# Kernel optimization log

Hardware: AMD Instinct MI355X
Metric: run time of the kernel (lower is better)

The kernel has to match this reference:

```python
import jax, jax.numpy as jnp
import numpy as np

V, D, DU, H = 50000, 256, 1024, 128
TEMP = 0.01

def time_cosine_emb(t, d_model):
    half = d_model // 2
    div_term = jnp.exp(jnp.arange(half, dtype=jnp.float32) * (-np.log(10000.0) / half))
    scaled = t[..., None] * div_term  # (B, L, half)
    return jnp.concatenate([jnp.sin(scaled), jnp.cos(scaled)], axis=-1)

def setup_inputs() -> dict:
    key = jax.random.key(0)
    ks = jax.random.split(key, 12)
    B, L = 64, 2048
    q_seq = jax.random.randint(ks[0], (B, L), 0, V)
    r_seq = jax.random.randint(ks[1], (B, L), 0, 3)
    t_seq = jax.random.uniform(ks[2], (B, L), dtype=jnp.float32) * 1000.0
    mask = jnp.ones((B, L), dtype=jnp.float32)
    q_tab = jax.random.normal(ks[3], (V, D), dtype=jnp.float32) * 0.02
    q_tab = q_tab.at[0].set(0.0)  # padding_idx=0
    r_tab = jax.random.normal(ks[4], (3, D), dtype=jnp.float32) * 0.02
    r_tab = r_tab.at[0].set(0.0)  # padding_idx=0
    virtual_node = jax.random.normal(ks[5], (1, D), dtype=jnp.float32)
    Ws1 = jax.random.normal(ks[6], (H, 2 * D), dtype=jnp.float32) * (1.0 / np.sqrt(2 * D))
    bs1 = jnp.zeros((H,), dtype=jnp.float32)
    Ws2 = jax.random.normal(ks[7], (1, H), dtype=jnp.float32) * (1.0 / np.sqrt(H))
    bs2 = jnp.zeros((1,), dtype=jnp.float32)
    Wa = jax.random.normal(ks[8], (DU, D), dtype=jnp.float32) * (1.0 / np.sqrt(D))
    ba = jnp.zeros((DU,), dtype=jnp.float32)
    return {"q_seq": q_seq, "r_seq": r_seq, "t_seq": t_seq, "mask": mask,
            "q_tab": q_tab, "r_tab": r_tab, "virtual_node": virtual_node,
            "Ws1": Ws1, "bs1": bs1, "Ws2": Ws2, "bs2": bs2, "Wa": Wa, "ba": ba}

def reference(q_seq, r_seq, t_seq, mask, q_tab, r_tab, virtual_node, Ws1, bs1, Ws2, bs2, Wa, ba):
    B, L = q_seq.shape
    d_model = q_tab.shape[1]
    # embedding gathers + trig time embedding
    h_events = q_tab[q_seq] + r_tab[r_seq] + time_cosine_emb(t_seq, d_model)  # (B,L,D)
    h_virtual = jnp.broadcast_to(virtual_node[None, :, :], (B, L, d_model))
    pair = jnp.concatenate([h_events, h_virtual], axis=-1)  # (B,L,2D)
    # struct_head: Linear -> LeakyReLU(0.2) -> Linear
    hdn = jax.nn.leaky_relu(jnp.einsum('bld,hd->blh', pair, Ws1) + bs1, 0.2)
    logits = jnp.einsum('blh,oh->blo', hdn, Ws2) + bs2  # (B,L,1)
    A_hat = jax.nn.sigmoid(logits / TEMP) * mask[..., None]
    # aggregator: Linear -> LeakyReLU(0.2)
    h_trans = jax.nn.leaky_relu(jnp.einsum('bld,ud->blu', h_events, Wa) + ba, 0.2)  # (B,L,DU)
    u_i = jnp.sum(h_trans * A_hat, axis=1)  # (B,DU)
    return (u_i, jnp.squeeze(A_hat, -1))
```

## Files before the change

kernel.cpp:

```cpp
#include <hip/hip_runtime.h>

typedef unsigned short ushort_t;
typedef unsigned int uint_t;

typedef short bf16x8 __attribute__((ext_vector_type(8)));
typedef float f32x4 __attribute__((ext_vector_type(4)));

#define MFMA16(a, b, c) __builtin_amdgcn_mfma_f32_16x16x32_bf16(a, b, c, 0, 0, 0)

__device__ __forceinline__ ushort_t f2bf(float f) {
    uint_t u = __float_as_uint(f);
    u += 0x7fffu + ((u >> 16) & 1u);
    return (ushort_t)(u >> 16);
}
__device__ __forceinline__ float bf2f(ushort_t h) {
    return __uint_as_float(((uint_t)h) << 16);
}

__device__ __forceinline__ void async16(const ushort_t* g, ushort_t* l) {
    __builtin_amdgcn_global_load_lds(
        (const __attribute__((address_space(1))) uint_t*)g,
        (__attribute__((address_space(3))) uint_t*)l, 16, 0, 0);
}

__global__ void k_prep(const float* __restrict__ Ws1, const float* __restrict__ bs1,
                       const float* __restrict__ virt, const float* __restrict__ Wa,
                       float* __restrict__ consth, ushort_t* __restrict__ wa_b,
                       ushort_t* __restrict__ ws1h, ushort_t* __restrict__ ws1l) {
    int b = blockIdx.x;
    if (b == 0) {
        int h = threadIdx.x;
        if (h < 128) {
            const float* row = Ws1 + h * 512 + 256;
            float s = bs1[h];
            for (int d = 0; d < 256; ++d) s += row[d] * virt[d];
            consth[h] = s;
        }
        return;
    }
    const float* src;
    int src_stride, tid;
    ushort_t *dhi, *dlo;
    if (b <= 128) {
        tid = (b - 1) * 256 + threadIdx.x;
        src = Wa; src_stride = 256; dhi = wa_b; dlo = nullptr;
    } else {
        tid = (b - 129) * 256 + threadIdx.x;
        src = Ws1; src_stride = 512; dhi = ws1h; dlo = ws1l;
    }
    int pl = tid & 15, kc = (tid >> 4) & 31, pt = tid >> 9;
    int row = pt * 16 + pl;
    const float* s = src + (size_t)row * src_stride + kc * 8;
    ushort_t hs[8], ls[8];
#pragma unroll
    for (int j = 0; j < 8; ++j) {
        float v = s[j];
        ushort_t h = f2bf(v);
        hs[j] = h;
        ls[j] = f2bf(v - bf2f(h));
    }
    uint4 hv;
    hv.x = hs[0] | ((uint_t)hs[1] << 16); hv.y = hs[2] | ((uint_t)hs[3] << 16);
    hv.z = hs[4] | ((uint_t)hs[5] << 16); hv.w = hs[6] | ((uint_t)hs[7] << 16);
    *(uint4*)(dhi + (size_t)tid * 8) = hv;
    if (dlo) {
        uint4 lv;
        lv.x = ls[0] | ((uint_t)ls[1] << 16); lv.y = ls[2] | ((uint_t)ls[3] << 16);
        lv.z = ls[4] | ((uint_t)ls[5] << 16); lv.w = ls[6] | ((uint_t)ls[7] << 16);
        *(uint4*)(dlo + (size_t)tid * 8) = lv;
    }
}

__global__ __launch_bounds__(256, 2) void k_embed_struct(
    const int* __restrict__ q_seq, const int* __restrict__ r_seq,
    const float* __restrict__ t_seq, const float* __restrict__ q_tab,
    const float* __restrict__ r_tab,
    const ushort_t* __restrict__ ws1h, const ushort_t* __restrict__ ws1l,
    const float* __restrict__ consth, const float* __restrict__ Ws2,
    const float* __restrict__ bs2, const float* __restrict__ mask,
    ushort_t* __restrict__ h_hi, float* __restrict__ out_ahat) {
    __shared__ __align__(16) char region[66560];
    __shared__ float sdiv[128];
    __shared__ float sLogit[64];
    ushort_t* sQ = (ushort_t*)region;
    ushort_t* sAhi = (ushort_t*)region;
    ushort_t* sAlo = (ushort_t*)(region + 32768);
    int tid = threadIdx.x;
    if (tid < 128) sdiv[tid] = __expf((float)tid * -0.07195578415606394f);
    if (tid < 64) sLogit[tid] = 0.0f;
    int w = tid >> 6, lane = tid & 63;
    int pl = lane & 15, kq = lane >> 4;
    int nl = pl;
    int p0 = blockIdx.x * 64;
    int p = p0 + w * 16 + pl;
    int qv = q_seq[p0 + w * 16 + pl];
    int rr = r_seq[p];
    float tt = t_seq[p];
#pragma unroll
    for (int i = 0; i < 16; ++i) {
        int row = __shfl(qv, i, 64);
        async16((const ushort_t*)(q_tab + (size_t)row * 256) + lane * 8,
                sQ + (w * 16 + i) * 520);
    }
    __syncthreads();
    uint4 hvA[8], lvA[8];
    const char* myrow = (const char*)sQ + (w * 16 + pl) * 1040;
    const float* rrow = r_tab + (size_t)rr * 256;
#pragma unroll
    for (int it = 0; it < 8; ++it) {
        int kc = it * 4 + kq;
        int k0 = kc * 8;
        float4 qa = *(const float4*)(myrow + kc * 32);
        float4 qb = *(const float4*)(myrow + kc * 32 + 16);
        float4 ra = *(const float4*)(rrow + kc * 8);
        float4 rb = *(const float4*)(rrow + kc * 8 + 4);
        float v[8] = {qa.x + ra.x, qa.y + ra.y, qa.z + ra.z, qa.w + ra.w,
                      qb.x + rb.x, qb.y + rb.y, qb.z + rb.z, qb.w + rb.w};
        bool iscos = (kc >= 16);
#pragma unroll
        for (int j = 0; j < 8; ++j) {
            float ang = tt * sdiv[(k0 + j) & 127];
            v[j] += iscos ? __cosf(ang) : __sinf(ang);
        }
        ushort_t hs[8], ls[8];
#pragma unroll
        for (int j = 0; j < 8; ++j) {
            ushort_t h = f2bf(v[j]);
            hs[j] = h;
            ls[j] = f2bf(v[j] - bf2f(h));
        }
        uint4 hv, lv;
        hv.x = hs[0] | ((uint_t)hs[1] << 16); hv.y = hs[2] | ((uint_t)hs[3] << 16);
        hv.z = hs[4] | ((uint_t)hs[5] << 16); hv.w = hs[6] | ((uint_t)hs[7] << 16);
        lv.x = ls[0] | ((uint_t)ls[1] << 16); lv.y = ls[2] | ((uint_t)ls[3] << 16);
        lv.z = ls[4] | ((uint_t)ls[5] << 16); lv.w = ls[6] | ((uint_t)ls[7] << 16);
        hvA[it] = hv; lvA[it] = lv;
        *(uint4*)(h_hi + ((size_t)((blockIdx.x * 4 + w) * 32 + kc) * 16 + pl) * 8) = hv;
    }
    __syncthreads();
#pragma unroll
    for (int it = 0; it < 8; ++it) {
        int kc = it * 4 + kq;
        int loff = ((w * 32 + kc) * 16 + pl) * 8;
        *(uint4*)(sAhi + loff) = hvA[it];
        *(uint4*)(sAlo + loff) = lvA[it];
    }
    __syncthreads();
    f32x4 acc[4][2];
    f32x4 z4 = {0.f, 0.f, 0.f, 0.f};
#pragma unroll
    for (int mt = 0; mt < 4; ++mt)
#pragma unroll
        for (int nt = 0; nt < 2; ++nt) acc[mt][nt] = z4;
    bf16x8 bhi[2], blo[2], nbhi[2], nblo[2];
#pragma unroll
    for (int nt = 0; nt < 2; ++nt) {
        int off = (((w * 2 + nt) * 32 + kq) * 16 + nl) * 8;
        bhi[nt] = *(const bf16x8*)(ws1h + off);
        blo[nt] = *(const bf16x8*)(ws1l + off);
    }
#pragma unroll 1
    for (int ks = 0; ks < 8; ++ks) {
        if (ks < 7) {
#pragma unroll
            for (int nt = 0; nt < 2; ++nt) {
                int off = (((w * 2 + nt) * 32 + (ks + 1) * 4 + kq) * 16 + nl) * 8;
                nbhi[nt] = *(const bf16x8*)(ws1h + off);
                nblo[nt] = *(const bf16x8*)(ws1l + off);
            }
        }
        bf16x8 ahi[4], alo[4];
#pragma unroll
        for (int mt = 0; mt < 4; ++mt) {
            int off = ((mt * 32 + ks * 4 + kq) * 16 + nl) * 8;
            ahi[mt] = *(const bf16x8*)&sAhi[off];
            alo[mt] = *(const bf16x8*)&sAlo[off];
        }
#pragma unroll
        for (int mt = 0; mt < 4; ++mt)
#pragma unroll
            for (int nt = 0; nt < 2; ++nt) {
                acc[mt][nt] = MFMA16(ahi[mt], bhi[nt], acc[mt][nt]);
                acc[mt][nt] = MFMA16(alo[mt], bhi[nt], acc[mt][nt]);
                acc[mt][nt] = MFMA16(ahi[mt], blo[nt], acc[mt][nt]);
            }
#pragma unroll
        for (int nt = 0; nt < 2; ++nt) { bhi[nt] = nbhi[nt]; blo[nt] = nblo[nt]; }
    }
    float ps[4][4];
#pragma unroll
    for (int mt = 0; mt < 4; ++mt)
#pragma unroll
        for (int r = 0; r < 4; ++r) ps[mt][r] = 0.f;
#pragma unroll
    for (int nt = 0; nt < 2; ++nt) {
        int ng = w * 32 + nt * 16 + nl;
        float chv = consth[ng], w2 = Ws2[ng];
#pragma unroll
        for (int mt = 0; mt < 4; ++mt)
#pragma unroll
            for (int r = 0; r < 4; ++r) {
                float v = acc[mt][nt][r] + chv;
                v = v > 0.f ? v : 0.2f * v;
                ps[mt][r] += v * w2;
            }
    }
#pragma unroll
    for (int mt = 0; mt < 4; ++mt)
#pragma unroll
        for (int r = 0; r < 4; ++r) {
            float x = ps[mt][r];
            x += __shfl_xor(x, 1, 64);
            x += __shfl_xor(x, 2, 64);
            x += __shfl_xor(x, 4, 64);
            x += __shfl_xor(x, 8, 64);
            ps[mt][r] = x;
        }
    if (nl == 0) {
#pragma unroll
        for (int mt = 0; mt < 4; ++mt)
#pragma unroll
            for (int r = 0; r < 4; ++r)
                atomicAdd(&sLogit[mt * 16 + kq * 4 + r], ps[mt][r]);
    }
    __syncthreads();
    if (tid < 64) {
        int pp = p0 + tid;
        float lg = sLogit[tid] + bs2[0];
        float y = lg * 100.0f;
        y = fminf(fmaxf(y, -60.f), 60.f);
        float a = 1.0f / (1.0f + expf(-y));
        out_ahat[pp] = a * mask[pp];
    }
}

__global__ __launch_bounds__(256, 2) void k_agg(
    const ushort_t* __restrict__ h_hi, const ushort_t* __restrict__ wa_blk,
    const float* __restrict__ ba, const float* __restrict__ ahat,
    float* __restrict__ u_i) {
    __shared__ float sAh[128];
    int tid = threadIdx.x;
    int w = tid >> 6, lane = tid & 63, nl = lane & 15, kq = lane >> 4;
    int p0 = blockIdx.x * 128, bidx = p0 >> 11;
    if (tid < 128) sAh[tid] = ahat[p0 + tid];
    int mh = w & 1, nh = w >> 1;
    bf16x8 afr[4][8];
    const ushort_t* gA = h_hi + (size_t)(p0 >> 4) * 4096;
#pragma unroll
    for (int mt = 0; mt < 4; ++mt) {
        const ushort_t* base = gA + (size_t)(mh * 4 + mt) * 4096;
#pragma unroll
        for (int ks = 0; ks < 8; ++ks)
            afr[mt][ks] = *(const bf16x8*)(base + ks * 512 + lane * 8);
    }
    __syncthreads();
    const ushort_t* gBw = wa_blk + (size_t)nh * 4 * 4096 + lane * 8;
#pragma unroll 1
    for (int nch = 0; nch < 8; ++nch) {
        const ushort_t* gB = gBw + (size_t)nch * 32768;
        f32x4 acc[4][4];
        bf16x8 bcur[4], bnxt[4];
#pragma unroll
        for (int nt = 0; nt < 4; ++nt)
            bcur[nt] = *(const bf16x8*)(gB + nt * 4096);
#pragma unroll
        for (int ks = 0; ks < 8; ++ks) {
            if (ks < 7) {
#pragma unroll
                for (int nt = 0; nt < 4; ++nt)
                    bnxt[nt] = *(const bf16x8*)(gB + nt * 4096 + (ks + 1) * 512);
            }
            if (ks == 0) {
                f32x4 z4 = {0.f, 0.f, 0.f, 0.f};
#pragma unroll
                for (int mt = 0; mt < 4; ++mt)
#pragma unroll
                    for (int nt = 0; nt < 4; ++nt)
                        acc[mt][nt] = MFMA16(afr[mt][0], bcur[nt], z4);
            } else {
#pragma unroll
                for (int mt = 0; mt < 4; ++mt)
#pragma unroll
                    for (int nt = 0; nt < 4; ++nt)
                        acc[mt][nt] = MFMA16(afr[mt][ks], bcur[nt], acc[mt][nt]);
            }
#pragma unroll
            for (int nt = 0; nt < 4; ++nt) bcur[nt] = bnxt[nt];
        }
        int n0 = nch * 128;
#pragma unroll
        for (int nt = 0; nt < 4; ++nt) {
            int ng = n0 + nh * 64 + nt * 16 + nl;
            float ban = ba[ng];
            float s = 0.f;
#pragma unroll
            for (int mt = 0; mt < 4; ++mt)
#pragma unroll
                for (int r = 0; r < 4; ++r) {
                    float v = acc[mt][nt][r] + ban;
                    v = v > 0.f ? v : 0.2f * v;
                    int ml = mh * 64 + mt * 16 + kq * 4 + r;
                    s += v * sAh[ml];
                }
            s += __shfl_xor(s, 16, 64);
            s += __shfl_xor(s, 32, 64);
            if (kq == 0) atomicAdd(&u_i[bidx * 1024 + ng], s);
        }
    }
}

extern "C" void kernel_launch(void* const* d_in, const int* in_sizes, int n_in,
                              void* d_out, int out_size, void* d_ws, size_t ws_size,
                              hipStream_t stream) {
    const int* q_seq = (const int*)d_in[0];
    const int* r_seq = (const int*)d_in[1];
    const float* t_seq = (const float*)d_in[2];
    const float* mask = (const float*)d_in[3];
    const float* q_tab = (const float*)d_in[4];
    const float* r_tab = (const float*)d_in[5];
    const float* virt = (const float*)d_in[6];
    const float* Ws1 = (const float*)d_in[7];
    const float* bs1 = (const float*)d_in[8];
    const float* Ws2 = (const float*)d_in[9];
    const float* bs2 = (const float*)d_in[10];
    const float* Wa = (const float*)d_in[11];
    const float* ba = (const float*)d_in[12];
    float* out = (float*)d_out;

    ushort_t* h_hi = (ushort_t*)d_ws;
    ushort_t* wa_b = h_hi + 33554432;
    ushort_t* ws1h = wa_b + 262144;
    ushort_t* ws1l = ws1h + 32768;
    float* ch = (float*)(ws1l + 32768);

    hipMemsetAsync(out, 0, 65536 * sizeof(float), stream);
    hipLaunchKernelGGL(k_prep, dim3(145), dim3(256), 0, stream,
                       Ws1, bs1, virt, Wa, ch, wa_b, ws1h, ws1l);
    hipLaunchKernelGGL(k_embed_struct, dim3(2048), dim3(256), 0, stream,
                       q_seq, r_seq, t_seq, q_tab, r_tab, ws1h, ws1l, ch, Ws2, bs2,
                       mask, h_hi, out + 65536);
    hipLaunchKernelGGL(k_agg, dim3(1024), dim3(256), 0, stream,
                       h_hi, wa_b, ba, out + 65536, out);
}
```

Baseline: 263.0 us.

## Fuse embedding/struct kernel with aggregator GEMM to drop h_hi round-trip

Merges the struct-head kernel and the aggregator kernel into one. The bf16 h_events tile now stays in shared memory and feeds the Wa GEMM directly, so the 64 MB h_hi intermediate is never written to or read back from global memory. Each 64-row block now runs all 1024 output columns, split across four waves. This doubles the number of Wa weight reads per row (64-row tiles instead of 128) and the atomics into u_i, and it makes each block longer with more register pressure. B-fragment prefetching is also changed from copy-swap to double-buffered arrays with the k-loop fully unrolled.

```diff
diff --git a/kernel.cpp b/kernel.cpp
--- a/kernel.cpp
+++ b/kernel.cpp
@@ -71,17 +71,19 @@
     }
 }
 
-__global__ __launch_bounds__(256, 2) void k_embed_struct(
+__global__ __launch_bounds__(256, 2) void k_fused(
     const int* __restrict__ q_seq, const int* __restrict__ r_seq,
     const float* __restrict__ t_seq, const float* __restrict__ q_tab,
     const float* __restrict__ r_tab,
     const ushort_t* __restrict__ ws1h, const ushort_t* __restrict__ ws1l,
     const float* __restrict__ consth, const float* __restrict__ Ws2,
     const float* __restrict__ bs2, const float* __restrict__ mask,
-    ushort_t* __restrict__ h_hi, float* __restrict__ out_ahat) {
+    const ushort_t* __restrict__ wa_b, const float* __restrict__ ba,
+    float* __restrict__ out_ahat, float* __restrict__ u_i) {
     __shared__ __align__(16) char region[66560];
     __shared__ float sdiv[128];
     __shared__ float sLogit[64];
+    __shared__ float sAh[64];
     ushort_t* sQ = (ushort_t*)region;
     ushort_t* sAhi = (ushort_t*)region;
     ushort_t* sAlo = (ushort_t*)(region + 32768);
@@ -93,7 +95,7 @@
     int nl = pl;
     int p0 = blockIdx.x * 64;
     int p = p0 + w * 16 + pl;
-    int qv = q_seq[p0 + w * 16 + pl];
+    int qv = q_seq[p];
     int rr = r_seq[p];
     float tt = t_seq[p];
 #pragma unroll
@@ -135,7 +137,6 @@
         lv.x = ls[0] | ((uint_t)ls[1] << 16); lv.y = ls[2] | ((uint_t)ls[3] << 16);
         lv.z = ls[4] | ((uint_t)ls[5] << 16); lv.w = ls[6] | ((uint_t)ls[7] << 16);
         hvA[it] = hv; lvA[it] = lv;
-        *(uint4*)(h_hi + ((size_t)((blockIdx.x * 4 + w) * 32 + kc) * 16 + pl) * 8) = hv;
     }
     __syncthreads();
 #pragma unroll
@@ -146,82 +147,83 @@
         *(uint4*)(sAlo + loff) = lvA[it];
     }
     __syncthreads();
-    f32x4 acc[4][2];
-    f32x4 z4 = {0.f, 0.f, 0.f, 0.f};
-#pragma unroll
-    for (int mt = 0; mt < 4; ++mt)
-#pragma unroll
-        for (int nt = 0; nt < 2; ++nt) acc[mt][nt] = z4;
-    bf16x8 bhi[2], blo[2], nbhi[2], nblo[2];
-#pragma unroll
-    for (int nt = 0; nt < 2; ++nt) {
-        int off = (((w * 2 + nt) * 32 + kq) * 16 + nl) * 8;
-        bhi[nt] = *(const bf16x8*)(ws1h + off);
-        blo[nt] = *(const bf16x8*)(ws1l + off);
-    }
-#pragma unroll 1
-    for (int ks = 0; ks < 8; ++ks) {
-        if (ks < 7) {
-#pragma unroll
-            for (int nt = 0; nt < 2; ++nt) {
-                int off = (((w * 2 + nt) * 32 + (ks + 1) * 4 + kq) * 16 + nl) * 8;
-                nbhi[nt] = *(const bf16x8*)(ws1h + off);
-                nblo[nt] = *(const bf16x8*)(ws1l + off);
-            }
-        }
-        bf16x8 ahi[4], alo[4];
-#pragma unroll
-        for (int mt = 0; mt < 4; ++mt) {
-            int off = ((mt * 32 + ks * 4 + kq) * 16 + nl) * 8;
-            ahi[mt] = *(const bf16x8*)&sAhi[off];
-            alo[mt] = *(const bf16x8*)&sAlo[off];
-        }
+    {
+        f32x4 acc[4][2];
+        f32x4 z4 = {0.f, 0.f, 0.f, 0.f};
 #pragma unroll
         for (int mt = 0; mt < 4; ++mt)
 #pragma unroll
-            for (int nt = 0; nt < 2; ++nt) {
-                acc[mt][nt] = MFMA16(ahi[mt], bhi[nt], acc[mt][nt]);
-                acc[mt][nt] = MFMA16(alo[mt], bhi[nt], acc[mt][nt]);
-                acc[mt][nt] = MFMA16(ahi[mt], blo[nt], acc[mt][nt]);
-            }
-#pragma unroll
-        for (int nt = 0; nt < 2; ++nt) { bhi[nt] = nbhi[nt]; blo[nt] = nblo[nt]; }
-    }
-    float ps[4][4];
-#pragma unroll
-    for (int mt = 0; mt < 4; ++mt)
-#pragma unroll
-        for (int r = 0; r < 4; ++r) ps[mt][r] = 0.f;
-#pragma unroll
-    for (int nt = 0; nt < 2; ++nt) {
-        int ng = w * 32 + nt * 16 + nl;
-        float chv = consth[ng], w2 = Ws2[ng];
+            for (int nt = 0; nt < 2; ++nt) acc[mt][nt] = z4;
+        bf16x8 bh[2][2], bl[2][2];
+#pragma unroll
+        for (int nt = 0; nt < 2; ++nt) {
+            int off = (((w * 2 + nt) * 32 + kq) * 16 + nl) * 8;
+            bh[0][nt] = *(const bf16x8*)(ws1h + off);
+            bl[0][nt] = *(const bf16x8*)(ws1l + off);
+        }
+#pragma unroll
+        for (int ks = 0; ks < 8; ++ks) {
+            int cur = ks & 1, nxt = cur ^ 1;
+            if (ks < 7) {
+#pragma unroll
+                for (int nt = 0; nt < 2; ++nt) {
+                    int off = (((w * 2 + nt) * 32 + (ks + 1) * 4 + kq) * 16 + nl) * 8;
+                    bh[nxt][nt] = *(const bf16x8*)(ws1h + off);
+                    bl[nxt][nt] = *(const bf16x8*)(ws1l + off);
+                }
+            }
+            bf16x8 ahi[4], alo[4];
+#pragma unroll
+            for (int mt = 0; mt < 4; ++mt) {
+                int off = ((mt * 32 + ks * 4 + kq) * 16 + nl) * 8;
+                ahi[mt] = *(const bf16x8*)&sAhi[off];
+                alo[mt] = *(const bf16x8*)&sAlo[off];
+            }
+#pragma unroll
+            for (int mt = 0; mt < 4; ++mt)
+#pragma unroll
+                for (int nt = 0; nt < 2; ++nt) {
+                    acc[mt][nt] = MFMA16(ahi[mt], bh[cur][nt], acc[mt][nt]);
+                    acc[mt][nt] = MFMA16(alo[mt], bh[cur][nt], acc[mt][nt]);
+                    acc[mt][nt] = MFMA16(ahi[mt], bl[cur][nt], acc[mt][nt]);
+                }
+        }
+        float ps[4][4];
 #pragma unroll
         for (int mt = 0; mt < 4; ++mt)
 #pragma unroll
+            for (int r = 0; r < 4; ++r) ps[mt][r] = 0.f;
+#pragma unroll
+        for (int nt = 0; nt < 2; ++nt) {
+            int ng = w * 32 + nt * 16 + nl;
+            float chv = consth[ng], w2 = Ws2[ng];
+#pragma unroll
+            for (int mt = 0; mt < 4; ++mt)
+#pragma unroll
+                for (int r = 0; r < 4; ++r) {
+                    float v = acc[mt][nt][r] + chv;
+                    v = v > 0.f ? v : 0.2f * v;
+                    ps[mt][r] += v * w2;
+                }
+        }
+#pragma unroll
+        for (int mt = 0; mt < 4; ++mt)
+#pragma unroll
             for (int r = 0; r < 4; ++r) {
-                float v = acc[mt][nt][r] + chv;
-                v = v > 0.f ? v : 0.2f * v;
-                ps[mt][r] += v * w2;
-            }
-    }
-#pragma unroll
-    for (int mt = 0; mt < 4; ++mt)
-#pragma unroll
-        for (int r = 0; r < 4; ++r) {
-            float x = ps[mt][r];
-            x += __shfl_xor(x, 1, 64);
-            x += __shfl_xor(x, 2, 64);
-            x += __shfl_xor(x, 4, 64);
-            x += __shfl_xor(x, 8, 64);
-            ps[mt][r] = x;
-        }
-    if (nl == 0) {
-#pragma unroll
-        for (int mt = 0; mt < 4; ++mt)
-#pragma unroll
-            for (int r = 0; r < 4; ++r)
-                atomicAdd(&sLogit[mt * 16 + kq * 4 + r], ps[mt][r]);
+                float x = ps[mt][r];
+                x += __shfl_xor(x, 1, 64);
+                x += __shfl_xor(x, 2, 64);
+                x += __shfl_xor(x, 4, 64);
+                x += __shfl_xor(x, 8, 64);
+                ps[mt][r] = x;
+            }
+        if (nl == 0) {
+#pragma unroll
+            for (int mt = 0; mt < 4; ++mt)
+#pragma unroll
+                for (int r = 0; r < 4; ++r)
+                    atomicAdd(&sLogit[mt * 16 + kq * 4 + r], ps[mt][r]);
+        }
     }
     __syncthreads();
     if (tid < 64) {
@@ -230,81 +232,68 @@
         float y = lg * 100.0f;
         y = fminf(fmaxf(y, -60.f), 60.f);
         float a = 1.0f / (1.0f + expf(-y));
-        out_ahat[pp] = a * mask[pp];
-    }
-}
-
-__global__ __launch_bounds__(256, 2) void k_agg(
-    const ushort_t* __restrict__ h_hi, const ushort_t* __restrict__ wa_blk,
-    const float* __restrict__ ba, const float* __restrict__ ahat,
-    float* __restrict__ u_i) {
-    __shared__ float sAh[128];
-    int tid = threadIdx.x;
-    int w = tid >> 6, lane = tid & 63, nl = lane & 15, kq = lane >> 4;
-    int p0 = blockIdx.x * 128, bidx = p0 >> 11;
-    if (tid < 128) sAh[tid] = ahat[p0 + tid];
-    int mh = w & 1, nh = w >> 1;
-    bf16x8 afr[4][8];
-    const ushort_t* gA = h_hi + (size_t)(p0 >> 4) * 4096;
-#pragma unroll
-    for (int mt = 0; mt < 4; ++mt) {
-        const ushort_t* base = gA + (size_t)(mh * 4 + mt) * 4096;
-#pragma unroll
-        for (int ks = 0; ks < 8; ++ks)
-            afr[mt][ks] = *(const bf16x8*)(base + ks * 512 + lane * 8);
-    }
-    __syncthreads();
-    const ushort_t* gBw = wa_blk + (size_t)nh * 4 * 4096 + lane * 8;
+        float av = a * mask[pp];
+        out_ahat[pp] = av;
+        sAh[tid] = av;
+    }
+    __syncthreads();
+    {
+        bf16x8 afr[4][8];
+#pragma unroll
+        for (int mt = 0; mt < 4; ++mt)
+#pragma unroll
+            for (int ks = 0; ks < 8; ++ks)
+                afr[mt][ks] = *(const bf16x8*)&sAhi[((mt * 32 + ks * 4 + kq) * 16 + nl) * 8];
+        int bidx = p0 >> 11;
 #pragma unroll 1
-    for (int nch = 0; nch < 8; ++nch) {
-        const ushort_t* gB = gBw + (size_t)nch * 32768;
-        f32x4 acc[4][4];
-        bf16x8 bcur[4], bnxt[4];
-#pragma unroll
-        for (int nt = 0; nt < 4; ++nt)
-            bcur[nt] = *(const bf16x8*)(gB + nt * 4096);
-#pragma unroll
-        for (int ks = 0; ks < 8; ++ks) {
-            if (ks < 7) {
-#pragma unroll
-                for (int nt = 0; nt < 4; ++nt)
-                    bnxt[nt] = *(const bf16x8*)(gB + nt * 4096 + (ks + 1) * 512);
-            }
-            if (ks == 0) {
-                f32x4 z4 = {0.f, 0.f, 0.f, 0.f};
+        for (int nblk = 0; nblk < 4; ++nblk) {
+            const ushort_t* gB = wa_b + (size_t)(w * 16 + nblk * 4) * 4096 + lane * 8;
+            f32x4 acc[4][4];
+            bf16x8 bfr[2][4];
+#pragma unroll
+            for (int nt = 0; nt < 4; ++nt)
+                bfr[0][nt] = *(const bf16x8*)(gB + nt * 4096);
+#pragma unroll
+            for (int ks = 0; ks < 8; ++ks) {
+                int cur = ks & 1, nxt = cur ^ 1;
+                if (ks < 7) {
+#pragma unroll
+                    for (int nt = 0; nt < 4; ++nt)
+                        bfr[nxt][nt] = *(const bf16x8*)(gB + nt * 4096 + (ks + 1) * 512);
+                }
+                if (ks == 0) {
+                    f32x4 z4 = {0.f, 0.f, 0.f, 0.f};
+#pragma unroll
+                    for (int mt = 0; mt < 4; ++mt)
+#pragma unroll
+                        for (int nt = 0; nt < 4; ++nt)
+                            acc[mt][nt] = MFMA16(afr[mt][0], bfr[0][nt], z4);
+                } else {
+#pragma unroll
+                    for (int mt = 0; mt < 4; ++mt)
+#pragma unroll
+                        for (int nt = 0; nt < 4; ++nt)
+                            acc[mt][nt] = MFMA16(afr[mt][ks], bfr[cur][nt], acc[mt][nt]);
+                }
+            }
+#pragma unroll
+            for (int nt = 0; nt < 4; ++nt) {
+                int ng = w * 256 + nblk * 64 + nt * 16 + nl;
+                float ban = ba[ng];
+                float s = 0.f;
 #pragma unroll
                 for (int mt = 0; mt < 4; ++mt)
 #pragma unroll
-                    for (int nt = 0; nt < 4; ++nt)
-                        acc[mt][nt] = MFMA16(afr[mt][0], bcur[nt], z4);
-            } else {
-#pragma unroll
-                for (int mt = 0; mt < 4; ++mt)
-#pragma unroll
-                    for (int nt = 0; nt < 4; ++nt)
-                        acc[mt][nt] = MFMA16(afr[mt][ks], bcur[nt], acc[mt][nt]);
-            }
-#pragma unroll
-            for (int nt = 0; nt < 4; ++nt) bcur[nt] = bnxt[nt];
-        }
-        int n0 = nch * 128;
-#pragma unroll
-        for (int nt = 0; nt < 4; ++nt) {
-            int ng = n0 + nh * 64 + nt * 16 + nl;
-            float ban = ba[ng];
-            float s = 0.f;
-#pragma unroll
-            for (int mt = 0; mt < 4; ++mt)
-#pragma unroll
-                for (int r = 0; r < 4; ++r) {
-                    float v = acc[mt][nt][r] + ban;
-                    v = v > 0.f ? v : 0.2f * v;
-                    int ml = mh * 64 + mt * 16 + kq * 4 + r;
-                    s += v * sAh[ml];
-                }
-            s += __shfl_xor(s, 16, 64);
-            s += __shfl_xor(s, 32, 64);
-            if (kq == 0) atomicAdd(&u_i[bidx * 1024 + ng], s);
+                    for (int r = 0; r < 4; ++r) {
+                        float v = acc[mt][nt][r] + ban;
+                        v = v > 0.f ? v : 0.2f * v;
+                        int ml = mt * 16 + kq * 4 + r;
+                        s += v * sAh[ml];
+                    }
+                s += __shfl_xor(s, 16, 64);
+                s += __shfl_xor(s, 32, 64);
+                if (kq == 0) atomicAdd(&u_i[bidx * 1024 + ng], s);
+            }
         }
     }
 }
@@ -327,8 +316,7 @@
     const float* ba = (const float*)d_in[12];
     float* out = (float*)d_out;
 
-    ushort_t* h_hi = (ushort_t*)d_ws;
-    ushort_t* wa_b = h_hi + 33554432;
+    ushort_t* wa_b = (ushort_t*)d_ws;
     ushort_t* ws1h = wa_b + 262144;
     ushort_t* ws1l = ws1h + 32768;
     float* ch = (float*)(ws1l + 32768);
@@ -336,9 +324,7 @@
     hipMemsetAsync(out, 0, 65536 * sizeof(float), stream);
     hipLaunchKernelGGL(k_prep, dim3(145), dim3(256), 0, stream,
                        Ws1, bs1, virt, Wa, ch, wa_b, ws1h, ws1l);
-    hipLaunchKernelGGL(k_embed_struct, dim3(2048), dim3(256), 0, stream,
+    hipLaunchKernelGGL(k_fused, dim3(2048), dim3(256), 0, stream,
                        q_seq, r_seq, t_seq, q_tab, r_tab, ws1h, ws1l, ch, Ws2, bs2,
-                       mask, h_hi, out + 65536);
-    hipLaunchKernelGGL(k_agg, dim3(1024), dim3(256), 0, stream,
-                       h_hi, wa_b, ba, out + 65536, out);
-}
+                       mask, wa_b, ba, out + 65536, out);
+}
```

Result: faster. 251.7 us (-4.3%).
